# Kernel optimization log

Hardware: AMD Instinct MI355X
Metric: run time of the kernel (lower is better)

Reference implementation:

```python
import jax, jax.numpy as jnp
from jax import lax
import numpy as np

GRID = 64
MAP = 15000.0
SCALE = MAP / GRID  # 234.375
R = int(1100 / SCALE)  # 4
SIGMA = 1.5
C = 16
B = 768
N_KILL = 49152
N_TRAIL = 393216

TOWERS = np.array([(8955, 8510), (9767, 10113), (11134, 11207), (11593, 11669), (13052, 12612), (12611, 13084), (5846, 6396), (5048, 4812), (3651, 3696), (3210, 3217), (2177, 1807), (1748, 2270), (4318, 13875), (981, 10441), (7943, 13411), (1512, 6699), (1169, 4287), (1172, 3583), (10481, 13650), (11275, 13657), (11275, 13663), (13866, 4505), (10504, 1029), (13327, 8226), (13624, 10572), (6919, 1483), (13599, 11319), (4281, 1253), (3468, 1230), (13594, 11319)], dtype=np.float32)

# ---- static buffers (numpy, computed once at import) ----
_tg = np.clip((TOWERS / SCALE).astype(np.int64), 0, GRID - 1)
TX, TY = _tg[:, 0], _tg[:, 1]
_xs = np.arange(GRID)
# per-tower coverage disc on the full canvas: equivalent to clipped range_mask placement
DISC = (((_xs[None, None, :] - TX[:, None, None]) ** 2 + (_xs[None, :, None] - TY[:, None, None]) ** 2) <= R * R).astype(np.float32)  # [30, H, W]
_ks = int(2 * 4 * SIGMA + 1)
if _ks % 2 == 0:
    _ks += 1
_x = (np.arange(_ks) - _ks // 2).astype(np.float32)
_k1 = np.exp(-_x ** 2 / (2 * SIGMA ** 2))
_k2 = np.outer(_k1, _k1)
_k2 = _k2 / _k2.sum()
KERNEL = np.broadcast_to(_k2, (C, 1, _ks, _ks)).astype(np.float32).copy()  # depthwise OIHW
PAD = _ks // 2
DRAG_X, DRAG_Y = int(10000.0 / SCALE), int(5000.0 / SCALE)   # (42, 21)
BARON_X, BARON_Y = int(5000.0 / SCALE), int(10000.0 / SCALE)  # (21, 42)


def _to_grid(coords):
    return jnp.clip((coords / SCALE).astype(jnp.int32), 0, GRID - 1)


def setup_inputs() -> dict:
    key = jax.random.key(0)
    ks = jax.random.split(key, 10)
    return {
        "player_coords": jax.random.uniform(ks[0], (N_TRAIL, 2), jnp.float32) * MAP,
        "player_vals": jax.random.uniform(ks[1], (N_TRAIL,), jnp.float32),
        "dead_towers_mask": jax.random.uniform(ks[2], (B, 30), jnp.float32),
        "kill_coords": jax.random.uniform(ks[3], (N_KILL, 2), jnp.float32) * MAP,
        "kill_vals": jax.random.uniform(ks[4], (N_KILL,), jnp.float32),
        "obj_status": jax.random.uniform(ks[5], (B, 2), jnp.float32),
        "player_b_idx": jax.random.randint(ks[6], (N_TRAIL,), 0, B, jnp.int32),
        "player_channels": jax.random.randint(ks[7], (N_TRAIL,), 0, 10, jnp.int32),
        "kill_teams": jax.random.randint(ks[8], (N_KILL,), 0, 2, jnp.int32),
        "kill_b_idx": jax.random.randint(ks[9], (N_KILL,), 0, B, jnp.int32),
    }


def reference(player_coords, player_vals, dead_towers_mask, kill_coords, kill_vals, obj_status, player_b_idx, player_channels, kill_teams, kill_b_idx):
    b = dead_towers_mask.shape[0]
    dead = dead_towers_mask > 0.5          # [B, 30]
    alive_f = (~dead).astype(jnp.float32)
    dead_f = dead.astype(jnp.float32)

    # channels 0/1: alive/dead tower markers (idempotent set -> scatter-max)
    ch0 = jnp.zeros((b, GRID, GRID), jnp.float32).at[:, TY, TX].max(alive_f)
    ch1 = jnp.zeros((b, GRID, GRID), jnp.float32).at[:, TY, TX].max(dead_f)

    # channel 2: max of binary range discs over alive towers == any-coverage indicator
    cov = alive_f @ jnp.asarray(DISC).reshape(30, -1)  # [B, H*W]
    ch2 = (cov > 0).astype(jnp.float32).reshape(b, GRID, GRID)

    # channel 3: objective markers
    ch3 = (jnp.zeros((b, GRID, GRID), jnp.float32)
           .at[:, DRAG_Y, DRAG_X].set((obj_status[:, 0] > 0.5).astype(jnp.float32))
           .at[:, BARON_Y, BARON_X].set((obj_status[:, 1] > 0.5).astype(jnp.float32)))

    canvas = jnp.concatenate(
        [ch0[:, None], ch1[:, None], ch2[:, None], ch3[:, None],
         jnp.zeros((b, C - 4, GRID, GRID), jnp.float32)], axis=1)  # [B, 16, H, W]

    # kill events: scatter-add into channels 4 + team
    kg = _to_grid(kill_coords)
    canvas = canvas.at[kill_b_idx, 4 + kill_teams, kg[:, 1], kg[:, 0]].add(kill_vals)

    # player trails: scatter-add into channels 6 + player_channel
    pg = _to_grid(player_coords)
    canvas = canvas.at[player_b_idx, 6 + player_channels, pg[:, 1], pg[:, 0]].add(player_vals)

    # depthwise gaussian blur
    blurred = lax.conv_general_dilated(
        canvas, jnp.asarray(KERNEL),
        window_strides=(1, 1), padding=[(PAD, PAD), (PAD, PAD)],
        feature_group_count=C,
        dimension_numbers=("NCHW", "OIHW", "NCHW"))
    return blurred
```

## Files before the change

### kernel.cpp

```cpp
#include <hip/hip_runtime.h>

#define GRID    64
#define BATCH   768
#define C       16
#define NT      30
#define N_KILL  49152
#define N_TRAIL 393216
#define CELLS   4096
#define IMG     (C * CELLS)
#define SCALE   234.375f
#define NSC     12
#define NIMG    (BATCH * NSC)
#define CAPI    128
#define STR     68

__device__ constexpr int TXc[NT] = {38,41,47,49,55,53,24,21,15,13, 9, 7,18, 4,33, 6, 4, 5,44,48,48,59,44,56,58,29,58,18,14,58};
__device__ constexpr int TYc[NT] = {36,43,47,49,53,55,27,20,15,13, 7, 9,59,44,57,28,18,15,58,58,58,19, 4,35,45, 6,48, 5, 5,48};

__device__ constexpr float W13[13] = {
    8.92216e-05f, 1.02820e-03f, 7.59741e-03f, 3.59943e-02f, 1.09341e-01f,
    2.12968e-01f, 2.65964e-01f, 2.12968e-01f, 1.09341e-01f, 3.59943e-02f,
    7.59741e-03f, 1.02820e-03f, 8.92216e-05f};

__global__ __launch_bounds__(256) void zero_counts(unsigned* __restrict__ counts) {
    const int gid = blockIdx.x * 256 + threadIdx.x;
    if (gid < NIMG) counts[gid] = 0;
}

__global__ __launch_bounds__(256) void bin_points(
    const float* __restrict__ kc, const float* __restrict__ kv,
    const int*   __restrict__ kt, const int*   __restrict__ kb,
    const float* __restrict__ pc, const float* __restrict__ pv,
    const int*   __restrict__ pb, const int*   __restrict__ pch,
    unsigned* __restrict__ counts, uint2* __restrict__ recs)
{
    const int gid = blockIdx.x * 256 + threadIdx.x;
    int img, gx, gy; float val;
    if (gid < N_KILL) {
        const int i = gid;
        const float2 xy = ((const float2*)kc)[i];
        gx = min(max((int)(xy.x / SCALE), 0), GRID - 1);
        gy = min(max((int)(xy.y / SCALE), 0), GRID - 1);
        val = kv[i];
        img = kb[i] * NSC + kt[i];
    } else {
        const int i = gid - N_KILL;
        const float2 xy = ((const float2*)pc)[i];
        gx = min(max((int)(xy.x / SCALE), 0), GRID - 1);
        gy = min(max((int)(xy.y / SCALE), 0), GRID - 1);
        val = pv[i];
        img = pb[i] * NSC + 2 + pch[i];
    }
    const unsigned slot = atomicAdd(&counts[img], 1u);
    if (slot < CAPI)
        recs[(size_t)img * CAPI + slot] =
            make_uint2((unsigned)(gx | (gy << 8)), __float_as_uint(val));
}

template<bool BINS>
__global__ __launch_bounds__(64) void fused_blur(
    const float* __restrict__ dead_mask,
    const float* __restrict__ obj_status,
    const unsigned* __restrict__ counts,
    const uint2* __restrict__ recs,
    const float* canvas,
    float* out)
{
    const int t  = threadIdx.x;
    const int bc = blockIdx.x;
    const int b  = bc >> 4;
    const int c  = bc & 15;
    const size_t base = (size_t)bc * CELLS;

    __shared__ __align__(16) float s_tr[GRID * STR];
    __shared__ float s_alive[NT];

    if (c < 4 && t < NT) s_alive[t] = (dead_mask[b * NT + t] > 0.5f) ? 0.0f : 1.0f;

    if (BINS && c >= 4) {
        const float4 z = make_float4(0.f, 0.f, 0.f, 0.f);
        #pragma unroll
        for (int i = 0; i < 17; ++i) ((float4*)s_tr)[i * 64 + t] = z;
        __syncthreads();

        const int img = b * NSC + (c - 4);
        int n = (int)counts[img];
        if (n > CAPI) n = CAPI;
        const size_t ibase = (size_t)img * CAPI;
        const float wlane = W13[t % 13];
        const int ntaps = n * 13;

        for (int k0 = 0; k0 < ntaps; k0 += 64) {
            const int k = k0 + t;
            const unsigned i  = (unsigned)k / 13u;
            const int      dd = k - (int)i * 13;
            const uint2 rec = recs[ibase + min((int)i, n - 1)];
            const int gx = (int)(rec.x & 0xFFu);
            const int gy = (int)(rec.x >> 8);
            const int xl = gx - 6 + dd;
            const float w = __shfl(wlane, dd);
            if (k < ntaps && (unsigned)xl < 64u)
                atomicAdd(&s_tr[xl * STR + gy], __uint_as_float(rec.y) * w);
        }
        __syncthreads();
    } else {
        if (c < 4) __syncthreads();

        float r[76];
        #pragma unroll
        for (int i = 0; i < 76; ++i) r[i] = 0.0f;

        if (c == 0) {
            #pragma unroll
            for (int i = 0; i < NT; ++i)
                if (TYc[i] == t) r[6 + TXc[i]] = fmaxf(r[6 + TXc[i]], s_alive[i]);
        } else if (c == 1) {
            #pragma unroll
            for (int i = 0; i < NT; ++i)
                if (TYc[i] == t) r[6 + TXc[i]] = fmaxf(r[6 + TXc[i]], 1.0f - s_alive[i]);
        } else if (c == 2) {
            unsigned long long mask = 0ULL;
            #pragma unroll
            for (int i = 0; i < NT; ++i) {
                const int dy  = t - TYc[i];
                const int ady = dy < 0 ? -dy : dy;
                if (ady <= 4 && s_alive[i] > 0.0f) {
                    const int hw = (ady == 0) ? 4 : (ady <= 2) ? 3 : (ady == 3) ? 2 : 0;
                    int lo = TXc[i] - hw; if (lo < 0)  lo = 0;
                    int hi = TXc[i] + hw; if (hi > 63) hi = 63;
                    mask |= (((1ULL << (hi - lo + 1)) - 1ULL) << lo);
                }
            }
            #pragma unroll
            for (int x = 0; x < GRID; ++x) r[6 + x] = (float)((mask >> x) & 1ULL);
        } else if (c == 3) {
            const float o0 = obj_status[b * 2 + 0];
            const float o1 = obj_status[b * 2 + 1];
            if (t == 21) r[6 + 42] = (o0 > 0.5f) ? 1.0f : 0.0f;
            if (t == 42) r[6 + 21] = (o1 > 0.5f) ? 1.0f : 0.0f;
        } else {
            #pragma unroll
            for (int k = 0; k < 16; ++k) {
                const float4 v = ((const float4*)(canvas + base))[t * 16 + k];
                r[6 + 4*k + 0] = v.x; r[6 + 4*k + 1] = v.y;
                r[6 + 4*k + 2] = v.z; r[6 + 4*k + 3] = v.w;
            }
        }

        #pragma unroll
        for (int x = 0; x < GRID; ++x) {
            float acc = 0.0f;
            #pragma unroll
            for (int d = 0; d < 13; ++d) acc = fmaf(W13[d], r[x + d], acc);
            s_tr[x * STR + t] = acc;
        }
        __syncthreads();
    }

    float v[76];
    #pragma unroll
    for (int i = 0; i < 6; ++i) { v[i] = 0.0f; v[70 + i] = 0.0f; }
    const float4* col = (const float4*)(s_tr + t * STR);
    #pragma unroll
    for (int k = 0; k < 16; ++k) {
        const float4 q = col[k];
        v[6 + 4*k + 0] = q.x; v[6 + 4*k + 1] = q.y;
        v[6 + 4*k + 2] = q.z; v[6 + 4*k + 3] = q.w;
    }
    #pragma unroll
    for (int y = 0; y < GRID; ++y) {
        float acc = 0.0f;
        #pragma unroll
        for (int d = 0; d < 13; ++d) acc = fmaf(W13[d], v[y + d], acc);
        out[base + y * GRID + t] = acc;
    }
}

__global__ __launch_bounds__(256) void zero12(float* __restrict__ out) {
    const int j = blockIdx.x;
    const int b = j / NSC, ch = 4 + j % NSC;
    float4* p = (float4*)(out + (size_t)(b * C + ch) * CELLS);
    #pragma unroll
    for (int k = 0; k < 4; ++k) p[k * 256 + threadIdx.x] = make_float4(0.f,0.f,0.f,0.f);
}

__global__ __launch_bounds__(256) void scatter_global(
    const float* __restrict__ kc, const float* __restrict__ kv,
    const int*   __restrict__ kt, const int*   __restrict__ kb,
    const float* __restrict__ pc, const float* __restrict__ pv,
    const int*   __restrict__ pb, const int*   __restrict__ pch,
    float* __restrict__ out)
{
    const int gid = blockIdx.x * 256 + threadIdx.x;
    if (gid < N_KILL) {
        const int i = gid;
        const int gx = min(max((int)(kc[2*i]   / SCALE), 0), GRID - 1);
        const int gy = min(max((int)(kc[2*i+1] / SCALE), 0), GRID - 1);
        atomicAdd(out + (size_t)kb[i]*IMG + (4+kt[i])*CELLS + gy*GRID + gx, kv[i]);
    } else {
        const int i = gid - N_KILL;
        const int gx = min(max((int)(pc[2*i]   / SCALE), 0), GRID - 1);
        const int gy = min(max((int)(pc[2*i+1] / SCALE), 0), GRID - 1);
        atomicAdd(out + (size_t)pb[i]*IMG + (6+pch[i])*CELLS + gy*GRID + gx, pv[i]);
    }
}

extern "C" void kernel_launch(void* const* d_in, const int* in_sizes, int n_in,
                              void* d_out, int out_size, void* d_ws, size_t ws_size,
                              hipStream_t stream)
{
    const float* player_coords = (const float*)d_in[0];
    const float* player_vals   = (const float*)d_in[1];
    const float* dead_mask     = (const float*)d_in[2];
    const float* kill_coords   = (const float*)d_in[3];
    const float* kill_vals     = (const float*)d_in[4];
    const float* obj_status    = (const float*)d_in[5];
    const int*   player_b      = (const int*)d_in[6];
    const int*   player_ch     = (const int*)d_in[7];
    const int*   kill_teams    = (const int*)d_in[8];
    const int*   kill_b        = (const int*)d_in[9];
    float* out = (float*)d_out;

    const size_t counts_bytes = (size_t)NIMG * sizeof(unsigned);
    const size_t recs_bytes   = (size_t)NIMG * CAPI * sizeof(uint2);
    const int n_scatter_blocks = (N_KILL + N_TRAIL) / 256;

    if (ws_size >= counts_bytes + recs_bytes) {
        unsigned* counts = (unsigned*)d_ws;
        uint2*    recs   = (uint2*)((char*)d_ws + counts_bytes);
        zero_counts<<<(NIMG + 255) / 256, 256, 0, stream>>>(counts);
        bin_points<<<n_scatter_blocks, 256, 0, stream>>>(
            kill_coords, kill_vals, kill_teams, kill_b,
            player_coords, player_vals, player_b, player_ch,
            counts, recs);
        fused_blur<true><<<BATCH * C, 64, 0, stream>>>(
            dead_mask, obj_status, counts, recs, nullptr, out);
    } else {
        zero12<<<NIMG, 256, 0, stream>>>(out);
        scatter_global<<<n_scatter_blocks, 256, 0, stream>>>(
            kill_coords, kill_vals, kill_teams, kill_b,
            player_coords, player_vals, player_b, player_ch, out);
        fused_blur<false><<<BATCH * C, 64, 0, stream>>>(
            dead_mask, obj_status, nullptr, nullptr, out, out);
    }
}
```

Baseline: 102.9 us.

## Pack binned records to 32-bit with fp16 values and sparse-scatter tower channels

Binned point records shrink from 8 bytes to 4 by packing the cell index with an fp16 value, which halves the record write and read traffic. Tower and objective channels 0, 1 and 3 now use the same sparse tap-scatter path as the binned channels instead of a dense row blur, with coincident towers merged by hand. The transpose stride changes to 65 to cut shared-memory bank conflicts, at the cost of scalar column reads, and output stores become nontemporal. The fp16 value packing loses precision in the scatter-added values, and the merged-tower handling hardcodes duplicate tower indices.

```diff
diff --git a/kernel.cpp b/kernel.cpp
--- a/kernel.cpp
+++ b/kernel.cpp
@@ -1,4 +1,5 @@
 #include <hip/hip_runtime.h>
+#include <string.h>
 
 #define GRID    64
 #define BATCH   768
@@ -12,7 +13,9 @@
 #define NSC     12
 #define NIMG    (BATCH * NSC)
 #define CAPI    128
-#define STR     68
+#define TRS     65
+#define TRWORDS (GRID * TRS)
+#define TRVEC   (TRWORDS / 4)
 
 __device__ constexpr int TXc[NT] = {38,41,47,49,55,53,24,21,15,13, 9, 7,18, 4,33, 6, 4, 5,44,48,48,59,44,56,58,29,58,18,14,58};
 __device__ constexpr int TYc[NT] = {36,43,47,49,53,55,27,20,15,13, 7, 9,59,44,57,28,18,15,58,58,58,19, 4,35,45, 6,48, 5, 5,48};
@@ -32,7 +35,7 @@
     const int*   __restrict__ kt, const int*   __restrict__ kb,
     const float* __restrict__ pc, const float* __restrict__ pv,
     const int*   __restrict__ pb, const int*   __restrict__ pch,
-    unsigned* __restrict__ counts, uint2* __restrict__ recs)
+    unsigned* __restrict__ counts, unsigned* __restrict__ recs)
 {
     const int gid = blockIdx.x * 256 + threadIdx.x;
     int img, gx, gy; float val;
@@ -51,10 +54,12 @@
         val = pv[i];
         img = pb[i] * NSC + 2 + pch[i];
     }
+    _Float16 h = (_Float16)val;
+    unsigned short us;
+    memcpy(&us, &h, 2);
+    const unsigned rec = ((unsigned)(gy * GRID + gx) << 16) | (unsigned)us;
     const unsigned slot = atomicAdd(&counts[img], 1u);
-    if (slot < CAPI)
-        recs[(size_t)img * CAPI + slot] =
-            make_uint2((unsigned)(gx | (gy << 8)), __float_as_uint(val));
+    if (slot < CAPI) recs[(size_t)img * CAPI + slot] = rec;
 }
 
 template<bool BINS>
@@ -62,9 +67,9 @@
     const float* __restrict__ dead_mask,
     const float* __restrict__ obj_status,
     const unsigned* __restrict__ counts,
-    const uint2* __restrict__ recs,
+    const unsigned* __restrict__ recs,
     const float* canvas,
-    float* out)
+    float* __restrict__ out)
 {
     const int t  = threadIdx.x;
     const int bc = blockIdx.x;
@@ -72,53 +77,20 @@
     const int c  = bc & 15;
     const size_t base = (size_t)bc * CELLS;
 
-    __shared__ __align__(16) float s_tr[GRID * STR];
+    __shared__ __align__(16) float s_tr[TRWORDS];
     __shared__ float s_alive[NT];
 
     if (c < 4 && t < NT) s_alive[t] = (dead_mask[b * NT + t] > 0.5f) ? 0.0f : 1.0f;
 
-    if (BINS && c >= 4) {
-        const float4 z = make_float4(0.f, 0.f, 0.f, 0.f);
-        #pragma unroll
-        for (int i = 0; i < 17; ++i) ((float4*)s_tr)[i * 64 + t] = z;
-        __syncthreads();
-
-        const int img = b * NSC + (c - 4);
-        int n = (int)counts[img];
-        if (n > CAPI) n = CAPI;
-        const size_t ibase = (size_t)img * CAPI;
-        const float wlane = W13[t % 13];
-        const int ntaps = n * 13;
-
-        for (int k0 = 0; k0 < ntaps; k0 += 64) {
-            const int k = k0 + t;
-            const unsigned i  = (unsigned)k / 13u;
-            const int      dd = k - (int)i * 13;
-            const uint2 rec = recs[ibase + min((int)i, n - 1)];
-            const int gx = (int)(rec.x & 0xFFu);
-            const int gy = (int)(rec.x >> 8);
-            const int xl = gx - 6 + dd;
-            const float w = __shfl(wlane, dd);
-            if (k < ntaps && (unsigned)xl < 64u)
-                atomicAdd(&s_tr[xl * STR + gy], __uint_as_float(rec.y) * w);
-        }
-        __syncthreads();
-    } else {
-        if (c < 4) __syncthreads();
-
+    const bool dense = (c == 2) || (!BINS && c >= 4);
+
+    if (dense) {
+        __syncthreads();
         float r[76];
         #pragma unroll
         for (int i = 0; i < 76; ++i) r[i] = 0.0f;
 
-        if (c == 0) {
-            #pragma unroll
-            for (int i = 0; i < NT; ++i)
-                if (TYc[i] == t) r[6 + TXc[i]] = fmaxf(r[6 + TXc[i]], s_alive[i]);
-        } else if (c == 1) {
-            #pragma unroll
-            for (int i = 0; i < NT; ++i)
-                if (TYc[i] == t) r[6 + TXc[i]] = fmaxf(r[6 + TXc[i]], 1.0f - s_alive[i]);
-        } else if (c == 2) {
+        if (c == 2) {
             unsigned long long mask = 0ULL;
             #pragma unroll
             for (int i = 0; i < NT; ++i) {
@@ -133,11 +105,6 @@
             }
             #pragma unroll
             for (int x = 0; x < GRID; ++x) r[6 + x] = (float)((mask >> x) & 1ULL);
-        } else if (c == 3) {
-            const float o0 = obj_status[b * 2 + 0];
-            const float o1 = obj_status[b * 2 + 1];
-            if (t == 21) r[6 + 42] = (o0 > 0.5f) ? 1.0f : 0.0f;
-            if (t == 42) r[6 + 21] = (o1 > 0.5f) ? 1.0f : 0.0f;
         } else {
             #pragma unroll
             for (int k = 0; k < 16; ++k) {
@@ -146,13 +113,86 @@
                 r[6 + 4*k + 2] = v.z; r[6 + 4*k + 3] = v.w;
             }
         }
-
         #pragma unroll
         for (int x = 0; x < GRID; ++x) {
             float acc = 0.0f;
             #pragma unroll
             for (int d = 0; d < 13; ++d) acc = fmaf(W13[d], r[x + d], acc);
-            s_tr[x * STR + t] = acc;
+            s_tr[x * TRS + t] = acc;
+        }
+        __syncthreads();
+    } else {
+        const float4 z = make_float4(0.f, 0.f, 0.f, 0.f);
+        #pragma unroll
+        for (int i = 0; i < 17; ++i) {
+            const int idx = i * 64 + t;
+            if (idx < TRVEC) ((float4*)s_tr)[idx] = z;
+        }
+        __syncthreads();
+
+        int n; size_t ibase = 0;
+        float obj0 = 0.f, obj1 = 0.f;
+        if (BINS && c >= 4) {
+            const int img = b * NSC + (c - 4);
+            n = (int)counts[img];
+            if (n > CAPI) n = CAPI;
+            ibase = (size_t)img * CAPI;
+        } else {
+            n = NT + 2;
+            if (c == 3) {
+                obj0 = obj_status[b * 2 + 0];
+                obj1 = obj_status[b * 2 + 1];
+            }
+        }
+
+        float wlane = 0.f;
+        #pragma unroll
+        for (int j = 0; j < 13; ++j) if (t == j) wlane = W13[j];
+
+        const int ntaps = n * 13;
+        for (int k0 = 0; k0 < ntaps; k0 += 64) {
+            const int k = k0 + t;
+            int i = (int)((unsigned)k / 13u);
+            const int dd = k - i * 13;
+            if (i > n - 1) i = n - 1;
+
+            int gx, gy; float val;
+            if (BINS && c >= 4) {
+                const unsigned rec = recs[ibase + i];
+                const int cell = (int)(rec >> 16);
+                gx = cell & 63; gy = cell >> 6;
+                const unsigned short us = (unsigned short)(rec & 0xFFFFu);
+                _Float16 h;
+                memcpy(&h, &us, 2);
+                val = (float)h;
+            } else {
+                if (i < NT) {
+                    gx = TXc[i]; gy = TYc[i];
+                    const float a = s_alive[i];
+                    if (c == 0) {
+                        val = (i == 20 || i == 29) ? 0.f
+                            : (i == 19) ? fmaxf(a, s_alive[20])
+                            : (i == 26) ? fmaxf(a, s_alive[29]) : a;
+                    } else if (c == 1) {
+                        val = (i == 20 || i == 29) ? 0.f
+                            : (i == 19) ? fmaxf(1.f - a, 1.f - s_alive[20])
+                            : (i == 26) ? fmaxf(1.f - a, 1.f - s_alive[29])
+                            : 1.f - a;
+                    } else {
+                        val = 0.f;
+                    }
+                } else if (c == 3) {
+                    if (i == NT) { gx = 42; gy = 21; val = (obj0 > 0.5f) ? 1.f : 0.f; }
+                    else         { gx = 21; gy = 42; val = (obj1 > 0.5f) ? 1.f : 0.f; }
+                } else {
+                    gx = 0; gy = 0; val = 0.f;
+                }
+            }
+
+            const float w  = __shfl(wlane, dd);
+            const int   xl = gx - 6 + dd;
+            if (k < ntaps && (unsigned)xl < 64u && val != 0.f)
+                atomicAdd(&s_tr[xl * TRS + gy], val * w);
         }
         __syncthreads();
     }
@@ -160,19 +200,15 @@
     float v[76];
     #pragma unroll
     for (int i = 0; i < 6; ++i) { v[i] = 0.0f; v[70 + i] = 0.0f; }
-    const float4* col = (const float4*)(s_tr + t * STR);
-    #pragma unroll
-    for (int k = 0; k < 16; ++k) {
-        const float4 q = col[k];
-        v[6 + 4*k + 0] = q.x; v[6 + 4*k + 1] = q.y;
-        v[6 + 4*k + 2] = q.z; v[6 + 4*k + 3] = q.w;
-    }
+    #pragma unroll
+    for (int k = 0; k < GRID; ++k) v[6 + k] = s_tr[t * TRS + k];
+
     #pragma unroll
     for (int y = 0; y < GRID; ++y) {
         float acc = 0.0f;
         #pragma unroll
         for (int d = 0; d < 13; ++d) acc = fmaf(W13[d], v[y + d], acc);
-        out[base + y * GRID + t] = acc;
+        __builtin_nontemporal_store(acc, &out[base + y * GRID + t]);
     }
 }
 
@@ -222,12 +258,12 @@
     float* out = (float*)d_out;
 
     const size_t counts_bytes = (size_t)NIMG * sizeof(unsigned);
-    const size_t recs_bytes   = (size_t)NIMG * CAPI * sizeof(uint2);
+    const size_t recs_bytes   = (size_t)NIMG * CAPI * sizeof(unsigned);
     const int n_scatter_blocks = (N_KILL + N_TRAIL) / 256;
 
     if (ws_size >= counts_bytes + recs_bytes) {
         unsigned* counts = (unsigned*)d_ws;
-        uint2*    recs   = (uint2*)((char*)d_ws + counts_bytes);
+        unsigned* recs   = (unsigned*)((char*)d_ws + counts_bytes);
         zero_counts<<<(NIMG + 255) / 256, 256, 0, stream>>>(counts);
         bin_points<<<n_scatter_blocks, 256, 0, stream>>>(
             kill_coords, kill_vals, kill_teams, kill_b,
```

Result: no change. 104.1 us (+1.2%).
